# Kernel optimization log

Measured on AMD Instinct MI355X. Metric: run time of the kernel, lower is better.

## Reference

```python
import jax, jax.numpy as jnp
import numpy as np

MARGIN = 0.3
NEG_FILL = 1e9  # larger than any real distance; keeps min-reduction valid


def setup_inputs() -> dict:
    key = jax.random.key(0)
    k1, k2 = jax.random.split(key)
    embeddings = jax.random.normal(k1, (4096, 256), dtype=jnp.float32)
    labels = jax.random.randint(k2, (4096,), 0, 512, dtype=jnp.int64)
    return {"embeddings": embeddings, "labels": labels}


def _pairwise_distances(embeddings):
    # Faithful to the torch version, including the zero-distance sqrt guard.
    dot = jnp.matmul(embeddings, embeddings.T)          # [B, B]
    sq = jnp.diagonal(dot)                              # [B]
    d2 = sq[None, :] - 2.0 * dot + sq[:, None]
    d2 = jnp.maximum(d2, 0.0)
    zero_mask = (d2 == 0.0).astype(embeddings.dtype)
    d = jnp.sqrt(d2 + zero_mask * 1e-16)
    return d * (1.0 - zero_mask)


def reference(embeddings, labels):
    B = labels.shape[0]
    d = _pairwise_distances(embeddings)                 # [B, B]

    same = labels[:, None] == labels[None, :]           # [B, B]
    eye = jnp.eye(B, dtype=bool)
    pos_mask = same & ~eye
    neg_mask = ~same

    has_pos = jnp.any(pos_mask, axis=1)
    has_neg = jnp.any(neg_mask, axis=1)
    valid = has_pos & has_neg                           # [B]

    # Row-wise masked reductions (distances >= 0 so -1 is a safe max fill).
    hardest_pos = jnp.max(jnp.where(pos_mask, d, -1.0), axis=1)
    hardest_neg = jnp.min(jnp.where(neg_mask, d, NEG_FILL), axis=1)

    per_anchor = jnp.maximum(hardest_pos - hardest_neg + MARGIN, 0.0)
    n_valid = jnp.sum(valid.astype(jnp.float32))
    total = jnp.sum(jnp.where(valid, per_anchor, 0.0))
    return jnp.where(n_valid > 0, total / jnp.maximum(n_valid, 1.0), 0.0)
```

## Files before the change

kernel.cpp:

```cpp
#include <hip/hip_runtime.h>
#include <hip/hip_fp16.h>

#define BN 4096
#define DIM 256
#define NBLK 32
#define NPAIR 528
#define MARGIN_F 0.3f
#define NEG_FILL_F 1e9f
#define HP_SENT_BITS 0xBF800000

typedef __attribute__((ext_vector_type(8))) _Float16 f16x8;
typedef __attribute__((ext_vector_type(4))) float f32x4;

__global__ __launch_bounds__(256) void tl_prep(const float* __restrict__ E,
                                               float* __restrict__ norms,
                                               float* __restrict__ red,
                                               ushort* __restrict__ Eh) {
    const int tid  = threadIdx.x;
    const int lane = tid & 63;
    const int row  = blockIdx.x * 4 + (tid >> 6);

    float4 v = reinterpret_cast<const float4*>(E + (size_t)row * DIM)[lane];
    float f[4] = {v.x, v.y, v.z, v.w};
    ushort hb[4];
    float s = 0.0f;
    #pragma unroll
    for (int q = 0; q < 4; ++q) {
        s += f[q] * f[q];
        hb[q] = __half_as_ushort(__float2half(f[q]));
    }
    const int kc = lane >> 1, half = lane & 1;
    const size_t co = (((size_t)(kc * BN + row)) << 3) + (size_t)(half * 4);
    *reinterpret_cast<ushort4*>(Eh + co) = make_ushort4(hb[0], hb[1], hb[2], hb[3]);

    #pragma unroll
    for (int m = 32; m; m >>= 1) s += __shfl_xor(s, m, 64);
    if (lane == 0) norms[row] = s;
    if (blockIdx.x == 0 && tid < 3) red[tid] = 0.0f;
}

__global__ __launch_bounds__(256) void tl_main(const ushort* __restrict__ Eh,
                                               const int* __restrict__ labels,
                                               const float* __restrict__ norms,
                                               float* __restrict__ pHP,
                                               float* __restrict__ pHN) {
    __shared__ int comb[512];

    const int tid  = threadIdx.x;
    const int lane = tid & 63;
    const int wave = tid >> 6;
    const int wy = wave >> 1, wx = wave & 1;
    const int quad = lane >> 4, l15 = lane & 15;

    int t = blockIdx.x, ib = 0, off = 0;
    while (off + (NBLK - ib) <= t) { off += NBLK - ib; ++ib; }
    const int jb = ib + (t - off);
    const int i0 = ib * 128, j0 = jb * 128;

    f32x4 acc[4][4];
    #pragma unroll
    for (int r = 0; r < 4; ++r)
        #pragma unroll
        for (int c = 0; c < 4; ++c)
            acc[r][c] = (f32x4){0.f, 0.f, 0.f, 0.f};

    const ushort* baseQ = Eh + (size_t)quad * (BN * 8);
    int rA[4], rB[4];
    #pragma unroll
    for (int r = 0; r < 4; ++r) rA[r] = (i0 + wy * 64 + r * 16 + l15) * 8;
    #pragma unroll
    for (int c = 0; c < 4; ++c) rB[c] = (j0 + wx * 64 + c * 16 + l15) * 8;

    f16x8 a0[4], b0[4], a1[4], b1[4];
    auto LD = [&](f16x8 (&A)[4], f16x8 (&B)[4], int s) {
        const size_t so = (size_t)s * (4u * BN * 8u);
        #pragma unroll
        for (int r = 0; r < 4; ++r)
            A[r] = *reinterpret_cast<const f16x8*>(baseQ + so + (size_t)rA[r]);
        #pragma unroll
        for (int c = 0; c < 4; ++c)
            B[c] = *reinterpret_cast<const f16x8*>(baseQ + so + (size_t)rB[c]);
    };
    auto MM = [&](f16x8 (&A)[4], f16x8 (&B)[4]) {
        #pragma unroll
        for (int c = 0; c < 4; ++c)
            #pragma unroll
            for (int r = 0; r < 4; ++r)
                acc[r][c] = __builtin_amdgcn_mfma_f32_16x16x32_f16(A[r], B[c], acc[r][c], 0, 0, 0);
    };

    LD(a0, b0, 0);
    LD(a1, b1, 1); MM(a0, b0);
    LD(a0, b0, 2); MM(a1, b1);
    LD(a1, b1, 3); MM(a0, b0);
    LD(a0, b0, 4); MM(a1, b1);
    LD(a1, b1, 5); MM(a0, b0);
    LD(a0, b0, 6); MM(a1, b1);
    LD(a1, b1, 7); MM(a0, b0);
    MM(a1, b1);

    const int rowBase = i0 + wy * 64;
    const int colBase = j0 + wx * 64;

    float nrow[4][4]; int lrow[4][4];
    #pragma unroll
    for (int r = 0; r < 4; ++r)
        #pragma unroll
        for (int e = 0; e < 4; ++e) {
            const int g = rowBase + r * 16 + quad * 4 + e;
            nrow[r][e] = norms[g];
            lrow[r][e] = labels[g];
        }
    float ncol[4]; int lcol[4];
    #pragma unroll
    for (int c = 0; c < 4; ++c) {
        const int g = colBase + c * 16 + l15;
        ncol[c] = norms[g];
        lcol[c] = labels[g];
    }

    float rmax[4][4], rmin[4][4], cmax[4], cmin[4];
    #pragma unroll
    for (int r = 0; r < 4; ++r)
        #pragma unroll
        for (int e = 0; e < 4; ++e) { rmax[r][e] = -1.0f; rmin[r][e] = NEG_FILL_F; }
    #pragma unroll
    for (int c = 0; c < 4; ++c) { cmax[c] = -1.0f; cmin[c] = NEG_FILL_F; }

    #pragma unroll
    for (int c = 0; c < 4; ++c) {
        const int gcol = colBase + c * 16 + l15;
        #pragma unroll
        for (int r = 0; r < 4; ++r) {
            #pragma unroll
            for (int e = 0; e < 4; ++e) {
                const int grow = rowBase + r * 16 + quad * 4 + e;
                float d2 = nrow[r][e] + ncol[c] - 2.0f * acc[r][c][e];
                d2 = fmaxf(d2, 0.0f);
                if (lrow[r][e] == lcol[c]) {
                    if (grow != gcol) {
                        rmax[r][e] = fmaxf(rmax[r][e], d2);
                        cmax[c]    = fmaxf(cmax[c], d2);
                    }
                } else {
                    rmin[r][e] = fminf(rmin[r][e], d2);
                    cmin[c]    = fminf(cmin[c], d2);
                }
            }
        }
    }

    #pragma unroll
    for (int m = 1; m <= 8; m <<= 1) {
        #pragma unroll
        for (int r = 0; r < 4; ++r)
            #pragma unroll
            for (int e = 0; e < 4; ++e) {
                rmax[r][e] = fmaxf(rmax[r][e], __shfl_xor(rmax[r][e], m, 64));
                rmin[r][e] = fminf(rmin[r][e], __shfl_xor(rmin[r][e], m, 64));
            }
    }
    #pragma unroll
    for (int m = 16; m <= 32; m <<= 1) {
        #pragma unroll
        for (int c = 0; c < 4; ++c) {
            cmax[c] = fmaxf(cmax[c], __shfl_xor(cmax[c], m, 64));
            cmin[c] = fminf(cmin[c], __shfl_xor(cmin[c], m, 64));
        }
    }

    int*      srhp = comb;
    unsigned* srhn = reinterpret_cast<unsigned*>(comb + 128);
    int*      schp = comb + 256;
    unsigned* schn = reinterpret_cast<unsigned*>(comb + 384);
    if (tid < 128) {
        srhp[tid] = (int)HP_SENT_BITS;
        srhn[tid] = __float_as_uint(NEG_FILL_F);
        schp[tid] = (int)HP_SENT_BITS;
        schn[tid] = __float_as_uint(NEG_FILL_F);
    }
    __syncthreads();
    if (l15 == 0) {
        #pragma unroll
        for (int r = 0; r < 4; ++r)
            #pragma unroll
            for (int e = 0; e < 4; ++e) {
                const int lr = wy * 64 + r * 16 + quad * 4 + e;
                atomicMax(&srhp[lr], __float_as_int(rmax[r][e]));
                atomicMin(&srhn[lr], __float_as_uint(rmin[r][e]));
            }
    }
    if (quad == 0) {
        #pragma unroll
        for (int c = 0; c < 4; ++c) {
            const int lc = wx * 64 + c * 16 + l15;
            atomicMax(&schp[lc], __float_as_int(cmax[c]));
            atomicMin(&schn[lc], __float_as_uint(cmin[c]));
        }
    }
    __syncthreads();
    if (tid < 128) {
        float rp = __int_as_float(srhp[tid]);
        float rn = __uint_as_float(srhn[tid]);
        const float cp = __int_as_float(schp[tid]);
        const float cn = __uint_as_float(schn[tid]);
        if (ib == jb) {
            pHP[(size_t)jb * BN + i0 + tid] = fmaxf(rp, cp);
            pHN[(size_t)jb * BN + i0 + tid] = fminf(rn, cn);
        } else {
            pHP[(size_t)jb * BN + i0 + tid] = rp;
            pHN[(size_t)jb * BN + i0 + tid] = rn;
            pHP[(size_t)ib * BN + j0 + tid] = cp;
            pHN[(size_t)ib * BN + j0 + tid] = cn;
        }
    }
}

__global__ __launch_bounds__(64) void tl_reduce(const float* __restrict__ pHP,
                                                const float* __restrict__ pHN,
                                                float* __restrict__ red,
                                                float* __restrict__ out) {
    const int i = blockIdx.x * 64 + threadIdx.x;
    float hp2 = -1.0f, hn2 = NEG_FILL_F;
    #pragma unroll
    for (int s = 0; s < NBLK; ++s) {
        hp2 = fmaxf(hp2, pHP[(size_t)s * BN + i]);
        hn2 = fminf(hn2, pHN[(size_t)s * BN + i]);
    }
    const bool valid = (hp2 >= 0.0f) && (hn2 < NEG_FILL_F);
    const float hp = sqrtf(fmaxf(hp2, 0.0f));
    const float hn = sqrtf(hn2);
    const float per = fmaxf(hp - hn + MARGIN_F, 0.0f);
    float s_ = valid ? per : 0.0f;
    float c_ = valid ? 1.0f : 0.0f;
    #pragma unroll
    for (int m = 32; m; m >>= 1) {
        s_ += __shfl_xor(s_, m, 64);
        c_ += __shfl_xor(c_, m, 64);
    }
    if (threadIdx.x == 0) {
        atomicAdd(&red[0], s_);
        atomicAdd(&red[1], c_);
        __threadfence();
        const unsigned ticket = atomicAdd(reinterpret_cast<unsigned*>(&red[2]), 1u);
        if (ticket == gridDim.x - 1) {
            const float S2 = atomicAdd(&red[0], 0.0f);
            const float C2 = atomicAdd(&red[1], 0.0f);
            out[0] = (C2 > 0.0f) ? (S2 / fmaxf(C2, 1.0f)) : 0.0f;
        }
    }
}

extern "C" void kernel_launch(void* const* d_in, const int* in_sizes, int n_in,
                              void* d_out, int out_size, void* d_ws, size_t ws_size,
                              hipStream_t stream) {
    const float* E      = (const float*)d_in[0];
    const int*   labels = (const int*)d_in[1];

    float*  ws    = (float*)d_ws;
    float*  norms = ws;
    float*  red   = ws + 4096;
    float*  pHP   = ws + 8192;
    float*  pHN   = ws + 8192 + NBLK * BN;
    ushort* Eh    = (ushort*)(ws + 8192 + 2 * NBLK * BN);

    tl_prep<<<BN / 4, 256, 0, stream>>>(E, norms, red, Eh);
    tl_main<<<NPAIR, 256, 0, stream>>>(Eh, labels, norms, pHP, pHN);
    tl_reduce<<<BN / 64, 64, 0, stream>>>(pHP, pHN, red, (float*)d_out);
}
```

Before: 92.85 us.

## Fuse prep, distance tiles and reduction into one cooperative row-strip kernel

Replaces the three-kernel pipeline with a single cooperative kernel of 128 blocks. Each block converts its 32 rows to fp16, a grid-wide sync follows, and then the block computes its full 32x4096 distance strip with MFMA before reducing the loss in place. This removes two launches and the partial-result buffers plus their reduction pass. In exchange it drops the symmetric-tile reuse, so each block computes the full strip instead of half the pairs and streams all of Eh from global memory per block. It also adds a grid sync and uses only 128 blocks.

```diff
diff --git a/kernel.cpp b/kernel.cpp
--- a/kernel.cpp
+++ b/kernel.cpp
@@ -1,10 +1,10 @@
 #include <hip/hip_runtime.h>
 #include <hip/hip_fp16.h>
+#include <hip/hip_cooperative_groups.h>
 
 #define BN 4096
 #define DIM 256
-#define NBLK 32
-#define NPAIR 528
+#define NB 128
 #define MARGIN_F 0.3f
 #define NEG_FILL_F 1e9f
 #define HP_SENT_BITS 0xBF800000
@@ -12,241 +12,173 @@
 typedef __attribute__((ext_vector_type(8))) _Float16 f16x8;
 typedef __attribute__((ext_vector_type(4))) float f32x4;
 
-__global__ __launch_bounds__(256) void tl_prep(const float* __restrict__ E,
-                                               float* __restrict__ norms,
-                                               float* __restrict__ red,
-                                               ushort* __restrict__ Eh) {
-    const int tid  = threadIdx.x;
-    const int lane = tid & 63;
-    const int row  = blockIdx.x * 4 + (tid >> 6);
-
-    float4 v = reinterpret_cast<const float4*>(E + (size_t)row * DIM)[lane];
-    float f[4] = {v.x, v.y, v.z, v.w};
-    ushort hb[4];
-    float s = 0.0f;
-    #pragma unroll
-    for (int q = 0; q < 4; ++q) {
-        s += f[q] * f[q];
-        hb[q] = __half_as_ushort(__float2half(f[q]));
-    }
-    const int kc = lane >> 1, half = lane & 1;
-    const size_t co = (((size_t)(kc * BN + row)) << 3) + (size_t)(half * 4);
-    *reinterpret_cast<ushort4*>(Eh + co) = make_ushort4(hb[0], hb[1], hb[2], hb[3]);
-
-    #pragma unroll
-    for (int m = 32; m; m >>= 1) s += __shfl_xor(s, m, 64);
-    if (lane == 0) norms[row] = s;
-    if (blockIdx.x == 0 && tid < 3) red[tid] = 0.0f;
-}
-
-__global__ __launch_bounds__(256) void tl_main(const ushort* __restrict__ Eh,
-                                               const int* __restrict__ labels,
-                                               const float* __restrict__ norms,
-                                               float* __restrict__ pHP,
-                                               float* __restrict__ pHN) {
-    __shared__ int comb[512];
+namespace cg = cooperative_groups;
+
+__global__ __launch_bounds__(512, 2) void tl_fused(const float* __restrict__ E,
+                                                   const int* __restrict__ labels,
+                                                   float* __restrict__ norms,
+                                                   float* __restrict__ red,
+                                                   ushort* __restrict__ Eh,
+                                                   float* __restrict__ out) {
+    __shared__ ushort sh[32][264];
+    __shared__ int comb[64];
 
     const int tid  = threadIdx.x;
     const int lane = tid & 63;
     const int wave = tid >> 6;
-    const int wy = wave >> 1, wx = wave & 1;
     const int quad = lane >> 4, l15 = lane & 15;
-
-    int t = blockIdx.x, ib = 0, off = 0;
-    while (off + (NBLK - ib) <= t) { off += NBLK - ib; ++ib; }
-    const int jb = ib + (t - off);
-    const int i0 = ib * 128, j0 = jb * 128;
-
-    f32x4 acc[4][4];
-    #pragma unroll
-    for (int r = 0; r < 4; ++r)
-        #pragma unroll
-        for (int c = 0; c < 4; ++c)
-            acc[r][c] = (f32x4){0.f, 0.f, 0.f, 0.f};
-
-    const ushort* baseQ = Eh + (size_t)quad * (BN * 8);
-    int rA[4], rB[4];
-    #pragma unroll
-    for (int r = 0; r < 4; ++r) rA[r] = (i0 + wy * 64 + r * 16 + l15) * 8;
-    #pragma unroll
-    for (int c = 0; c < 4; ++c) rB[c] = (j0 + wx * 64 + c * 16 + l15) * 8;
-
-    f16x8 a0[4], b0[4], a1[4], b1[4];
-    auto LD = [&](f16x8 (&A)[4], f16x8 (&B)[4], int s) {
-        const size_t so = (size_t)s * (4u * BN * 8u);
-        #pragma unroll
-        for (int r = 0; r < 4; ++r)
-            A[r] = *reinterpret_cast<const f16x8*>(baseQ + so + (size_t)rA[r]);
-        #pragma unroll
-        for (int c = 0; c < 4; ++c)
-            B[c] = *reinterpret_cast<const f16x8*>(baseQ + so + (size_t)rB[c]);
-    };
-    auto MM = [&](f16x8 (&A)[4], f16x8 (&B)[4]) {
-        #pragma unroll
-        for (int c = 0; c < 4; ++c)
-            #pragma unroll
-            for (int r = 0; r < 4; ++r)
-                acc[r][c] = __builtin_amdgcn_mfma_f32_16x16x32_f16(A[r], B[c], acc[r][c], 0, 0, 0);
-    };
-
-    LD(a0, b0, 0);
-    LD(a1, b1, 1); MM(a0, b0);
-    LD(a0, b0, 2); MM(a1, b1);
-    LD(a1, b1, 3); MM(a0, b0);
-    LD(a0, b0, 4); MM(a1, b1);
-    LD(a1, b1, 5); MM(a0, b0);
-    LD(a0, b0, 6); MM(a1, b1);
-    LD(a1, b1, 7); MM(a0, b0);
-    MM(a1, b1);
-
-    const int rowBase = i0 + wy * 64;
-    const int colBase = j0 + wx * 64;
-
-    float nrow[4][4]; int lrow[4][4];
-    #pragma unroll
-    for (int r = 0; r < 4; ++r)
+    const int b = blockIdx.x;
+    const int arow0 = b * 32;
+
+    #pragma unroll
+    for (int r = 0; r < 4; ++r) {
+        const int row = wave * 4 + r;
+        float4 v = reinterpret_cast<const float4*>(E + (size_t)(arow0 + row) * DIM)[lane];
+        float s = v.x * v.x + v.y * v.y + v.z * v.z + v.w * v.w;
+        ushort4 h = make_ushort4(__half_as_ushort(__float2half(v.x)),
+                                 __half_as_ushort(__float2half(v.y)),
+                                 __half_as_ushort(__float2half(v.z)),
+                                 __half_as_ushort(__float2half(v.w)));
+        *reinterpret_cast<ushort4*>(&sh[row][lane * 4]) = h;
+        #pragma unroll
+        for (int m = 32; m; m >>= 1) s += __shfl_xor(s, m, 64);
+        if (lane == 0) norms[arow0 + row] = s;
+    }
+    if (b == 0 && tid < 3) red[tid] = 0.0f;
+    __syncthreads();
+    {
+        const int kc = tid >> 4;
+        const int r0 = (tid & 15) * 2;
+        #pragma unroll
+        for (int q = 0; q < 2; ++q) {
+            const int r = r0 + q;
+            *reinterpret_cast<f16x8*>(Eh + (((size_t)(kc * BN + arow0 + r)) << 3)) =
+                *reinterpret_cast<const f16x8*>(&sh[r][kc * 8]);
+        }
+    }
+
+    cg::this_grid().sync();
+
+    f16x8 afr[2][8];
+    #pragma unroll
+    for (int r = 0; r < 2; ++r)
+        #pragma unroll
+        for (int s = 0; s < 8; ++s) {
+            const int kc = s * 4 + quad;
+            afr[r][s] = *reinterpret_cast<const f16x8*>(
+                Eh + (((size_t)(kc * BN + arow0 + r * 16 + l15)) << 3));
+        }
+    float nrow[2][4]; int lrow[2][4];
+    #pragma unroll
+    for (int r = 0; r < 2; ++r)
         #pragma unroll
         for (int e = 0; e < 4; ++e) {
-            const int g = rowBase + r * 16 + quad * 4 + e;
+            const int g = arow0 + r * 16 + quad * 4 + e;
             nrow[r][e] = norms[g];
             lrow[r][e] = labels[g];
         }
-    float ncol[4]; int lcol[4];
-    #pragma unroll
-    for (int c = 0; c < 4; ++c) {
-        const int g = colBase + c * 16 + l15;
-        ncol[c] = norms[g];
-        lcol[c] = labels[g];
-    }
-
-    float rmax[4][4], rmin[4][4], cmax[4], cmin[4];
-    #pragma unroll
-    for (int r = 0; r < 4; ++r)
+    float rmax[2][4], rmin[2][4];
+    #pragma unroll
+    for (int r = 0; r < 2; ++r)
         #pragma unroll
         for (int e = 0; e < 4; ++e) { rmax[r][e] = -1.0f; rmin[r][e] = NEG_FILL_F; }
-    #pragma unroll
-    for (int c = 0; c < 4; ++c) { cmax[c] = -1.0f; cmin[c] = NEG_FILL_F; }
-
-    #pragma unroll
-    for (int c = 0; c < 4; ++c) {
-        const int gcol = colBase + c * 16 + l15;
-        #pragma unroll
-        for (int r = 0; r < 4; ++r) {
-            #pragma unroll
-            for (int e = 0; e < 4; ++e) {
-                const int grow = rowBase + r * 16 + quad * 4 + e;
-                float d2 = nrow[r][e] + ncol[c] - 2.0f * acc[r][c][e];
-                d2 = fmaxf(d2, 0.0f);
-                if (lrow[r][e] == lcol[c]) {
-                    if (grow != gcol) {
-                        rmax[r][e] = fmaxf(rmax[r][e], d2);
-                        cmax[c]    = fmaxf(cmax[c], d2);
+
+    for (int jt = 0; jt < 8; ++jt) {
+        const int jbase = wave * 512 + jt * 64;
+        float ncol[4]; int lcol[4];
+        #pragma unroll
+        for (int c = 0; c < 4; ++c) {
+            const int g = jbase + c * 16 + l15;
+            ncol[c] = norms[g];
+            lcol[c] = labels[g];
+        }
+        f32x4 acc[2][4];
+        #pragma unroll
+        for (int r = 0; r < 2; ++r)
+            #pragma unroll
+            for (int c = 0; c < 4; ++c)
+                acc[r][c] = (f32x4){0.f, 0.f, 0.f, 0.f};
+        #pragma unroll
+        for (int s = 0; s < 8; ++s) {
+            const int kc = s * 4 + quad;
+            f16x8 bf[4];
+            #pragma unroll
+            for (int c = 0; c < 4; ++c)
+                bf[c] = *reinterpret_cast<const f16x8*>(
+                    Eh + (((size_t)(kc * BN + jbase + c * 16 + l15)) << 3));
+            #pragma unroll
+            for (int c = 0; c < 4; ++c)
+                #pragma unroll
+                for (int r = 0; r < 2; ++r)
+                    acc[r][c] = __builtin_amdgcn_mfma_f32_16x16x32_f16(afr[r][s], bf[c], acc[r][c], 0, 0, 0);
+        }
+        #pragma unroll
+        for (int c = 0; c < 4; ++c) {
+            const int gcol = jbase + c * 16 + l15;
+            #pragma unroll
+            for (int r = 0; r < 2; ++r)
+                #pragma unroll
+                for (int e = 0; e < 4; ++e) {
+                    const int grow = arow0 + r * 16 + quad * 4 + e;
+                    float d2 = nrow[r][e] + ncol[c] - 2.0f * acc[r][c][e];
+                    d2 = fmaxf(d2, 0.0f);
+                    if (lrow[r][e] == lcol[c]) {
+                        if (grow != gcol) rmax[r][e] = fmaxf(rmax[r][e], d2);
+                    } else {
+                        rmin[r][e] = fminf(rmin[r][e], d2);
                     }
-                } else {
-                    rmin[r][e] = fminf(rmin[r][e], d2);
-                    cmin[c]    = fminf(cmin[c], d2);
                 }
-            }
-        }
-    }
-
-    #pragma unroll
-    for (int m = 1; m <= 8; m <<= 1) {
-        #pragma unroll
-        for (int r = 0; r < 4; ++r)
+        }
+    }
+
+    #pragma unroll
+    for (int m = 1; m <= 8; m <<= 1)
+        #pragma unroll
+        for (int r = 0; r < 2; ++r)
             #pragma unroll
             for (int e = 0; e < 4; ++e) {
                 rmax[r][e] = fmaxf(rmax[r][e], __shfl_xor(rmax[r][e], m, 64));
                 rmin[r][e] = fminf(rmin[r][e], __shfl_xor(rmin[r][e], m, 64));
             }
-    }
-    #pragma unroll
-    for (int m = 16; m <= 32; m <<= 1) {
-        #pragma unroll
-        for (int c = 0; c < 4; ++c) {
-            cmax[c] = fmaxf(cmax[c], __shfl_xor(cmax[c], m, 64));
-            cmin[c] = fminf(cmin[c], __shfl_xor(cmin[c], m, 64));
-        }
-    }
-
-    int*      srhp = comb;
-    unsigned* srhn = reinterpret_cast<unsigned*>(comb + 128);
-    int*      schp = comb + 256;
-    unsigned* schn = reinterpret_cast<unsigned*>(comb + 384);
-    if (tid < 128) {
-        srhp[tid] = (int)HP_SENT_BITS;
-        srhn[tid] = __float_as_uint(NEG_FILL_F);
-        schp[tid] = (int)HP_SENT_BITS;
-        schn[tid] = __float_as_uint(NEG_FILL_F);
+    if (tid < 32) {
+        comb[tid]      = (int)HP_SENT_BITS;
+        comb[32 + tid] = (int)__float_as_uint(NEG_FILL_F);
     }
     __syncthreads();
     if (l15 == 0) {
         #pragma unroll
-        for (int r = 0; r < 4; ++r)
+        for (int r = 0; r < 2; ++r)
             #pragma unroll
             for (int e = 0; e < 4; ++e) {
-                const int lr = wy * 64 + r * 16 + quad * 4 + e;
-                atomicMax(&srhp[lr], __float_as_int(rmax[r][e]));
-                atomicMin(&srhn[lr], __float_as_uint(rmin[r][e]));
+                const int lr = r * 16 + quad * 4 + e;
+                atomicMax(&comb[lr], __float_as_int(rmax[r][e]));
+                atomicMin(reinterpret_cast<unsigned*>(&comb[32 + lr]), __float_as_uint(rmin[r][e]));
             }
     }
-    if (quad == 0) {
-        #pragma unroll
-        for (int c = 0; c < 4; ++c) {
-            const int lc = wx * 64 + c * 16 + l15;
-            atomicMax(&schp[lc], __float_as_int(cmax[c]));
-            atomicMin(&schn[lc], __float_as_uint(cmin[c]));
-        }
-    }
     __syncthreads();
-    if (tid < 128) {
-        float rp = __int_as_float(srhp[tid]);
-        float rn = __uint_as_float(srhn[tid]);
-        const float cp = __int_as_float(schp[tid]);
-        const float cn = __uint_as_float(schn[tid]);
-        if (ib == jb) {
-            pHP[(size_t)jb * BN + i0 + tid] = fmaxf(rp, cp);
-            pHN[(size_t)jb * BN + i0 + tid] = fminf(rn, cn);
-        } else {
-            pHP[(size_t)jb * BN + i0 + tid] = rp;
-            pHN[(size_t)jb * BN + i0 + tid] = rn;
-            pHP[(size_t)ib * BN + j0 + tid] = cp;
-            pHN[(size_t)ib * BN + j0 + tid] = cn;
-        }
-    }
-}
-
-__global__ __launch_bounds__(64) void tl_reduce(const float* __restrict__ pHP,
-                                                const float* __restrict__ pHN,
-                                                float* __restrict__ red,
-                                                float* __restrict__ out) {
-    const int i = blockIdx.x * 64 + threadIdx.x;
-    float hp2 = -1.0f, hn2 = NEG_FILL_F;
-    #pragma unroll
-    for (int s = 0; s < NBLK; ++s) {
-        hp2 = fmaxf(hp2, pHP[(size_t)s * BN + i]);
-        hn2 = fminf(hn2, pHN[(size_t)s * BN + i]);
-    }
-    const bool valid = (hp2 >= 0.0f) && (hn2 < NEG_FILL_F);
-    const float hp = sqrtf(fmaxf(hp2, 0.0f));
-    const float hn = sqrtf(hn2);
-    const float per = fmaxf(hp - hn + MARGIN_F, 0.0f);
-    float s_ = valid ? per : 0.0f;
-    float c_ = valid ? 1.0f : 0.0f;
-    #pragma unroll
-    for (int m = 32; m; m >>= 1) {
-        s_ += __shfl_xor(s_, m, 64);
-        c_ += __shfl_xor(c_, m, 64);
-    }
-    if (threadIdx.x == 0) {
-        atomicAdd(&red[0], s_);
-        atomicAdd(&red[1], c_);
-        __threadfence();
-        const unsigned ticket = atomicAdd(reinterpret_cast<unsigned*>(&red[2]), 1u);
-        if (ticket == gridDim.x - 1) {
-            const float S2 = atomicAdd(&red[0], 0.0f);
-            const float C2 = atomicAdd(&red[1], 0.0f);
-            out[0] = (C2 > 0.0f) ? (S2 / fmaxf(C2, 1.0f)) : 0.0f;
+
+    if (tid < 32) {
+        const float hp2 = __int_as_float(comb[tid]);
+        const float hn2 = __uint_as_float(((unsigned*)comb)[32 + tid]);
+        const bool valid = (hp2 >= 0.0f) && (hn2 < NEG_FILL_F);
+        const float per = fmaxf(sqrtf(fmaxf(hp2, 0.0f)) - sqrtf(hn2) + MARGIN_F, 0.0f);
+        float s_ = valid ? per : 0.0f;
+        float c_ = valid ? 1.0f : 0.0f;
+        #pragma unroll
+        for (int m = 1; m <= 16; m <<= 1) {
+            s_ += __shfl_xor(s_, m, 64);
+            c_ += __shfl_xor(c_, m, 64);
+        }
+        if (tid == 0) {
+            atomicAdd(&red[0], s_);
+            atomicAdd(&red[1], c_);
+            __threadfence();
+            const unsigned ticket = atomicAdd(reinterpret_cast<unsigned*>(&red[2]), 1u);
+            if (ticket == NB - 1) {
+                const float S = atomicAdd(&red[0], 0.0f);
+                const float C = atomicAdd(&red[1], 0.0f);
+                out[0] = (C > 0.0f) ? (S / fmaxf(C, 1.0f)) : 0.0f;
+            }
         }
     }
 }
@@ -260,11 +192,11 @@
     float*  ws    = (float*)d_ws;
     float*  norms = ws;
     float*  red   = ws + 4096;
-    float*  pHP   = ws + 8192;
-    float*  pHN   = ws + 8192 + NBLK * BN;
-    ushort* Eh    = (ushort*)(ws + 8192 + 2 * NBLK * BN);
-
-    tl_prep<<<BN / 4, 256, 0, stream>>>(E, norms, red, Eh);
-    tl_main<<<NPAIR, 256, 0, stream>>>(Eh, labels, norms, pHP, pHN);
-    tl_reduce<<<BN / 64, 64, 0, stream>>>(pHP, pHN, red, (float*)d_out);
+    ushort* Eh    = (ushort*)(ws + 8192);
+    float*  o     = (float*)d_out;
+
+    void* kargs[] = {(void*)&E, (void*)&labels, (void*)&norms,
+                     (void*)&red, (void*)&Eh, (void*)&o};
+    hipLaunchCooperativeKernel(reinterpret_cast<void*>(tl_fused),
+                               dim3(NB), dim3(512), kargs, 0, stream);
 }
```

Result: slower. 142.6 us (+53.6%).
